# Performance work log

Measured on AMD Instinct MI355X. Metric: run time of the kernel, lower is better.

Reference implementation:

```python
import jax, jax.numpy as jnp
import numpy as np

V, E, H, Z, T = 8185, 353, 191, 13, 25
START = 19


def _lstm(x, h, c, k, rk, b):
    # Keras LSTMCell: gates ordered i, f, g(candidate), o
    gates = x @ k + h @ rk + b                      # (B, 4H)
    i, f, g, o = jnp.split(gates, 4, axis=-1)
    c_new = jax.nn.sigmoid(f) * c + jax.nn.sigmoid(i) * jnp.tanh(g)
    h_new = jax.nn.sigmoid(o) * jnp.tanh(c_new)
    return h_new, c_new


def setup_inputs() -> dict:
    key = jax.random.key(0)
    ks = jax.random.split(key, 18)
    B = 256
    s = 0.05
    inp = {
        "inputs": jax.random.randint(ks[0], (B, T), 0, V),
        "epsilon": jax.random.normal(ks[1], (Z,), jnp.float32),
        "emb": jax.random.normal(ks[2], (V, E), jnp.float32) * s,
        "inf_k": jax.random.normal(ks[3], (E, 4 * H), jnp.float32) * s,
        "inf_rk": jax.random.normal(ks[4], (H, 4 * H), jnp.float32) * s,
        "inf_b": jnp.zeros((4 * H,), jnp.float32),
        "mu_w": jax.random.normal(ks[5], (H, Z), jnp.float32) * s,
        "mu_b": jnp.zeros((Z,), jnp.float32),
        "sig_w": jax.random.normal(ks[6], (H, Z), jnp.float32) * s,
        "sig_b": jnp.zeros((Z,), jnp.float32),
        "init_w": jax.random.normal(ks[7], (Z, H), jnp.float32) * s,
        "init_b": jnp.zeros((H,), jnp.float32),
        "gen_k": jax.random.normal(ks[8], (E, 4 * H), jnp.float32) * s,
        "gen_rk": jax.random.normal(ks[9], (H, 4 * H), jnp.float32) * s,
        "gen_b": jnp.zeros((4 * H,), jnp.float32),
        "out_w": jax.random.normal(ks[10], (H, V), jnp.float32) * s,
        "out_b": jnp.zeros((V,), jnp.float32),
    }
    return inp


def reference(inputs, epsilon, emb, inf_k, inf_rk, inf_b, mu_w, mu_b,
              sig_w, sig_b, init_w, init_b, gen_k, gen_rk, gen_b,
              out_w, out_b):
    B = inputs.shape[0]
    # ----- encoder (inference LSTM over the full sequence) -----
    inf_emb = emb[inputs]                             # (B, T, E)

    def enc_step(carry, x_t):
        h, c = carry
        h, c = _lstm(x_t, h, c, inf_k, inf_rk, inf_b)
        return (h, c), None

    h0 = jnp.zeros((B, H), emb.dtype)
    (h_enc, _), _ = jax.lax.scan(enc_step, (h0, h0),
                                 jnp.swapaxes(inf_emb, 0, 1))  # scan over T

    mu = h_enc @ mu_w + mu_b                          # (B, Z)
    sigma = h_enc @ sig_w + sig_b                     # (B, Z)
    z = mu + epsilon * sigma                          # shared epsilon (Z,)

    init_state = z @ init_w + init_b                  # (B, H)
    emb0 = jnp.broadcast_to(emb[START], (B, E))       # start token embedding

    def dec_step(carry, _):
        h, c, x = carry
        h, c = _lstm(x, h, c, gen_k, gen_rk, gen_b)
        logits = h @ out_w + out_b                    # (B, V)
        new_ind = jnp.argmax(logits, axis=-1)         # (B,)
        x_next = emb[new_ind]                         # (B, E)
        return (h, c, x_next), logits

    _, logits_seq = jax.lax.scan(dec_step, (init_state, init_state, emb0),
                                 None, length=T)      # (T, B, V)
    return jnp.swapaxes(logits_seq, 0, 1)             # (B, T, V)
```

## Files before the change

kernel.cpp:

```cpp
#include <hip/hip_runtime.h>
#include <math.h>

#define V_  8185
#define E_  353
#define H_  191
#define FH_ 764
#define Z_  13
#define T_  25
#define START_ 19
#define VP_ 8192
#define NT_ 32

__device__ __forceinline__ float sigf(float x) { return 1.0f / (1.0f + expf(-x)); }

__global__ __launch_bounds__(256) void pad_w_kernel(const float* __restrict__ src,
                                                    float* __restrict__ dst) {
  int i = blockIdx.x * 256 + threadIdx.x;
  if (i >= H_ * VP_) return;
  int k = i >> 13;
  int j = i & (VP_ - 1);
  dst[i] = (j < V_) ? src[(size_t)k * V_ + j] : 0.0f;
}

__global__ __launch_bounds__(256) void gemm_ew(const float* __restrict__ emb,
                                               const float* __restrict__ W,
                                               float* __restrict__ C, int M,
                                               const int* __restrict__ inputs,
                                               int mode, int B) {
  __shared__ __align__(16) float AT[E_ * 16];
  const int tid = threadIdx.x;
  const int n0 = blockIdx.x * 256;
  const int m0 = blockIdx.y * 16;
  for (int i = tid; i < 16 * E_; i += 256) {
    int r = i / E_, k = i - r * E_;
    int m = m0 + r;
    float v = 0.0f;
    if (m < M) {
      int row;
      if (mode == 0) row = m;
      else { int t = m / B, b = m - t * B; row = inputs[b * T_ + t]; }
      v = emb[(size_t)row * E_ + k];
    }
    AT[k * 16 + r] = v;
  }
  __syncthreads();
  const int lane = tid & 63;
  const int w4 = (tid >> 6) * 4;
  const int j = n0 + lane * 4;
  if (j >= FH_) return;
  float4 c0 = {0,0,0,0}, c1 = {0,0,0,0}, c2 = {0,0,0,0}, c3 = {0,0,0,0};
  const float* wc = W + j;
  const float* at = AT + w4;
  for (int k = 0; k < E_; ++k) {
    float4 wv = *(const float4*)(wc + (size_t)k * FH_);
    float4 a  = *(const float4*)(at + k * 16);
    c0.x = fmaf(a.x, wv.x, c0.x); c0.y = fmaf(a.x, wv.y, c0.y);
    c0.z = fmaf(a.x, wv.z, c0.z); c0.w = fmaf(a.x, wv.w, c0.w);
    c1.x = fmaf(a.y, wv.x, c1.x); c1.y = fmaf(a.y, wv.y, c1.y);
    c1.z = fmaf(a.y, wv.z, c1.z); c1.w = fmaf(a.y, wv.w, c1.w);
    c2.x = fmaf(a.z, wv.x, c2.x); c2.y = fmaf(a.z, wv.y, c2.y);
    c2.z = fmaf(a.z, wv.z, c2.z); c2.w = fmaf(a.z, wv.w, c2.w);
    c3.x = fmaf(a.w, wv.x, c3.x); c3.y = fmaf(a.w, wv.y, c3.y);
    c3.z = fmaf(a.w, wv.z, c3.z); c3.w = fmaf(a.w, wv.w, c3.w);
  }
  const int mb = m0 + w4;
  if (mb + 0 < M) *(float4*)(C + (size_t)(mb + 0) * FH_ + j) = c0;
  if (mb + 1 < M) *(float4*)(C + (size_t)(mb + 1) * FH_ + j) = c1;
  if (mb + 2 < M) *(float4*)(C + (size_t)(mb + 2) * FH_ + j) = c2;
  if (mb + 3 < M) *(float4*)(C + (size_t)(mb + 3) * FH_ + j) = c3;
}

__global__ __launch_bounds__(256) void lstm_step(const float* __restrict__ xk,
                                                 const float* __restrict__ rk,
                                                 const float* __restrict__ bias,
                                                 const float* __restrict__ h_in,
                                                 const float* __restrict__ c_in,
                                                 float* __restrict__ h_out,
                                                 float* __restrict__ c_out,
                                                 const float* __restrict__ pmax,
                                                 const int* __restrict__ pidx,
                                                 int mode, int first) {
  __shared__ float hs[16 * H_];
  __shared__ float xs[16 * 32];
  __shared__ float bs[32];
  __shared__ int   tk[16];
  __shared__ float pv[16 * NT_];
  __shared__ int   pi[16 * NT_];
  __shared__ float gb[32 * 16];

  const int tid = threadIdx.x;
  const int c0 = blockIdx.x * 8;
  const int m0 = blockIdx.y * 16;

  if (mode) {
    if (first) {
      if (tid < 16) tk[tid] = START_;
    } else {
      for (int i = tid; i < 16 * NT_; i += 256) {
        int row = i >> 5, s = i & (NT_ - 1);
        pv[i] = pmax[(size_t)(m0 + row) * NT_ + s];
        pi[i] = pidx[(size_t)(m0 + row) * NT_ + s];
      }
      __syncthreads();
      if (tid < 16) {
        float bv = pv[tid * NT_]; int bi = pi[tid * NT_];
        for (int s = 1; s < NT_; ++s) {
          float v = pv[tid * NT_ + s]; int ii = pi[tid * NT_ + s];
          if (v > bv || (v == bv && ii < bi)) { bv = v; bi = ii; }
        }
        tk[tid] = bi;
      }
    }
    __syncthreads();
  }

  for (int i = tid; i < 16 * H_; i += 256) hs[i] = h_in[(size_t)m0 * H_ + i];
  for (int i = tid; i < 16 * 32; i += 256) {
    int row = i >> 5, q = i & 31;
    int jj = c0 + (q & 7);
    int jg = jj + H_ * (q >> 3);
    float xv = 0.0f;
    if (jj < H_) {
      const float* xrow = mode ? (xk + (size_t)tk[row] * FH_)
                               : (xk + (size_t)(m0 + row) * FH_);
      xv = xrow[jg];
    }
    xs[i] = xv;
  }
  if (tid < 32) {
    int jj = c0 + (tid & 7);
    bs[tid] = (jj < H_) ? bias[jj + H_ * (tid >> 3)] : 0.0f;
  }
  __syncthreads();

  const int q = tid & 31, rg = tid >> 5;
  const int jj = c0 + (q & 7);
  const int jg = jj + H_ * (q >> 3);
  float a0 = 0.0f, a1 = 0.0f;
  if (jj < H_) {
    const float* rkp = rk + jg;
    const float* h0p = hs + rg * H_;
    const float* h1p = hs + (rg + 8) * H_;
    for (int k = 0; k < H_; ++k) {
      float wv = rkp[(size_t)k * FH_];
      a0 = fmaf(h0p[k], wv, a0);
      a1 = fmaf(h1p[k], wv, a1);
    }
  }
  gb[q * 16 + rg] = a0;
  gb[q * 16 + rg + 8] = a1;
  __syncthreads();

  if (tid < 128) {
    int cc = tid & 7, row = tid >> 3;
    int jc = c0 + cc;
    if (jc < H_) {
      float gi = gb[(cc      ) * 16 + row] + xs[row * 32 + cc      ] + bs[cc];
      float gf = gb[( 8 + cc ) * 16 + row] + xs[row * 32 +  8 + cc ] + bs[ 8 + cc];
      float gg = gb[(16 + cc ) * 16 + row] + xs[row * 32 + 16 + cc ] + bs[16 + cc];
      float go = gb[(24 + cc ) * 16 + row] + xs[row * 32 + 24 + cc ] + bs[24 + cc];
      float co = c_in[(size_t)(m0 + row) * H_ + jc];
      float cn = sigf(gf) * co + sigf(gi) * tanhf(gg);
      float hn = sigf(go) * tanhf(cn);
      c_out[(size_t)(m0 + row) * H_ + jc] = cn;
      h_out[(size_t)(m0 + row) * H_ + jc] = hn;
    }
  }
}

__global__ __launch_bounds__(256) void logits_argmax(const float* __restrict__ h,
                                                     const float* __restrict__ wp,
                                                     const float* __restrict__ ob,
                                                     float* __restrict__ out, int t,
                                                     float* __restrict__ pmax,
                                                     int* __restrict__ pidx) {
  __shared__ __align__(16) float AT[H_ * 16];
  const int tid = threadIdx.x;
  const int n0 = blockIdx.x * 256;
  const int m0 = blockIdx.y * 16;
  for (int i = tid; i < 16 * H_; i += 256) {
    int r = i / H_, k = i - r * H_;
    AT[k * 16 + r] = h[(size_t)m0 * H_ + i];
  }
  __syncthreads();
  const int lane = tid & 63;
  const int w4 = (tid >> 6) * 4;
  const int j = n0 + lane * 4;
  float4 c0 = {0,0,0,0}, c1 = {0,0,0,0}, c2 = {0,0,0,0}, c3 = {0,0,0,0};
  const float* wc = wp + j;
  const float* at = AT + w4;
  for (int k = 0; k < H_; ++k) {
    float4 wv = *(const float4*)(wc + (size_t)k * VP_);
    float4 a  = *(const float4*)(at + k * 16);
    c0.x = fmaf(a.x, wv.x, c0.x); c0.y = fmaf(a.x, wv.y, c0.y);
    c0.z = fmaf(a.x, wv.z, c0.z); c0.w = fmaf(a.x, wv.w, c0.w);
    c1.x = fmaf(a.y, wv.x, c1.x); c1.y = fmaf(a.y, wv.y, c1.y);
    c1.z = fmaf(a.y, wv.z, c1.z); c1.w = fmaf(a.y, wv.w, c1.w);
    c2.x = fmaf(a.z, wv.x, c2.x); c2.y = fmaf(a.z, wv.y, c2.y);
    c2.z = fmaf(a.z, wv.z, c2.z); c2.w = fmaf(a.z, wv.w, c2.w);
    c3.x = fmaf(a.w, wv.x, c3.x); c3.y = fmaf(a.w, wv.y, c3.y);
    c3.z = fmaf(a.w, wv.z, c3.z); c3.w = fmaf(a.w, wv.w, c3.w);
  }
  float bias[4];
#pragma unroll
  for (int u = 0; u < 4; ++u) bias[u] = (j + u < V_) ? ob[j + u] : 0.0f;
  float4 accs[4] = {c0, c1, c2, c3};
  const int b0 = m0 + w4;
#pragma unroll
  for (int r = 0; r < 4; ++r) {
    const int b = b0 + r;
    float v[4] = {accs[r].x + bias[0], accs[r].y + bias[1],
                  accs[r].z + bias[2], accs[r].w + bias[3]};
    float* orow = out + ((size_t)b * T_ + t) * V_ + j;
#pragma unroll
    for (int u = 0; u < 4; ++u)
      if (j + u < V_) orow[u] = v[u];
    float bv = -INFINITY; int bi = 0;
#pragma unroll
    for (int u = 0; u < 4; ++u)
      if (j + u < V_ && v[u] > bv) { bv = v[u]; bi = j + u; }
#pragma unroll
    for (int off = 1; off < 64; off <<= 1) {
      float ov = __shfl_xor(bv, off, 64);
      int   oi = __shfl_xor(bi, off, 64);
      if (ov > bv || (ov == bv && oi < bi)) { bv = ov; bi = oi; }
    }
    if (lane == 0) {
      pmax[(size_t)b * NT_ + blockIdx.x] = bv;
      pidx[(size_t)b * NT_ + blockIdx.x] = bi;
    }
  }
}

__global__ __launch_bounds__(64) void latent_k(const float* __restrict__ h,
                                               const float* __restrict__ eps,
                                               const float* __restrict__ mu_w,
                                               const float* __restrict__ mu_b,
                                               const float* __restrict__ sig_w,
                                               const float* __restrict__ sig_b,
                                               const float* __restrict__ iw,
                                               const float* __restrict__ ib,
                                               float* __restrict__ h0,
                                               float* __restrict__ c0) {
  __shared__ float zs[4 * Z_];
  const int tid = threadIdx.x;
  const int m0 = blockIdx.x * 4;
  if (tid < 4 * Z_) {
    int row = tid / Z_, qz = tid - row * Z_;
    const float* hr = h + (size_t)(m0 + row) * H_;
    float mu = mu_b[qz], sg = sig_b[qz];
    for (int k = 0; k < H_; ++k) {
      float hv = hr[k];
      mu = fmaf(hv, mu_w[k * Z_ + qz], mu);
      sg = fmaf(hv, sig_w[k * Z_ + qz], sg);
    }
    zs[tid] = mu + eps[qz] * sg;
  }
  __syncthreads();
  for (int i = tid; i < 4 * H_; i += 64) {
    int row = i / H_, col = i - row * H_;
    float acc = ib[col];
#pragma unroll
    for (int qz = 0; qz < Z_; ++qz)
      acc = fmaf(zs[row * Z_ + qz], iw[qz * H_ + col], acc);
    h0[(size_t)(m0 + row) * H_ + col] = acc;
    c0[(size_t)(m0 + row) * H_ + col] = acc;
  }
}

extern "C" void kernel_launch(void* const* d_in, const int* in_sizes, int n_in,
                              void* d_out, int out_size, void* d_ws, size_t ws_size,
                              hipStream_t stream) {
  const int*   inputs = (const int*)  d_in[0];
  const float* eps    = (const float*)d_in[1];
  const float* emb    = (const float*)d_in[2];
  const float* inf_k  = (const float*)d_in[3];
  const float* inf_rk = (const float*)d_in[4];
  const float* inf_b  = (const float*)d_in[5];
  const float* mu_w   = (const float*)d_in[6];
  const float* mu_b   = (const float*)d_in[7];
  const float* sig_w  = (const float*)d_in[8];
  const float* sig_b  = (const float*)d_in[9];
  const float* init_w = (const float*)d_in[10];
  const float* init_b = (const float*)d_in[11];
  const float* gen_k  = (const float*)d_in[12];
  const float* gen_rk = (const float*)d_in[13];
  const float* gen_b  = (const float*)d_in[14];
  const float* out_w  = (const float*)d_in[15];
  const float* out_b  = (const float*)d_in[16];
  float* out = (float*)d_out;

  const int B = in_sizes[0] / T_;
  const int BH = B * H_;

  float* ws = (float*)d_ws;
  size_t off = 0;
  float* EK = ws + off; off += (size_t)V_ * FH_;
  float* XK = ws + off; off += (size_t)T_ * B * FH_;
  float* WP = ws + off; off += (size_t)H_ * VP_;
  float* hbase = ws + off; off += (size_t)8 * BH;
  float* he[2] = {hbase + 0 * BH, hbase + 2 * BH};
  float* ce[2] = {hbase + 1 * BH, hbase + 3 * BH};
  float* hd[2] = {hbase + 4 * BH, hbase + 6 * BH};
  float* cd[2] = {hbase + 5 * BH, hbase + 7 * BH};
  float* pmax = ws + off; off += (size_t)B * NT_;
  int*   pidx = (int*)(ws + off); off += (size_t)B * NT_;

  hipMemsetAsync(hbase, 0, (size_t)2 * BH * sizeof(float), stream);

  pad_w_kernel<<<(H_ * VP_ + 255) / 256, 256, 0, stream>>>(out_w, WP);
  gemm_ew<<<dim3(3, (V_ + 15) / 16), 256, 0, stream>>>(emb, gen_k, EK, V_, nullptr, 0, B);
  gemm_ew<<<dim3(3, (T_ * B) / 16), 256, 0, stream>>>(emb, inf_k, XK, T_ * B, inputs, 1, B);

  for (int t = 0; t < T_; ++t) {
    lstm_step<<<dim3(24, B / 16), 256, 0, stream>>>(
        XK + (size_t)t * B * FH_, inf_rk, inf_b,
        he[t & 1], ce[t & 1], he[(t + 1) & 1], ce[(t + 1) & 1],
        nullptr, nullptr, 0, 0);
  }

  latent_k<<<B / 4, 64, 0, stream>>>(he[T_ & 1], eps, mu_w, mu_b, sig_w, sig_b,
                                     init_w, init_b, hd[0], cd[0]);

  for (int t = 0; t < T_; ++t) {
    lstm_step<<<dim3(24, B / 16), 256, 0, stream>>>(
        EK, gen_rk, gen_b,
        hd[t & 1], cd[t & 1], hd[(t + 1) & 1], cd[(t + 1) & 1],
        pmax, pidx, 1, (t == 0) ? 1 : 0);
    logits_argmax<<<dim3(NT_, B / 16), 256, 0, stream>>>(
        hd[(t + 1) & 1], WP, out_b, out, t, pmax, pidx);
  }
}
```

Measured before the change: 1.889 ms.

## Fuse encoder timesteps and latent into one persistent kernel; retile GEMMs

Replaces the 25 per-step encoder launches and the latent kernel with a single encoder_all kernel. Each block runs the whole encoder recurrence for two batch rows with h/c kept in shared memory, then computes mu/sigma/z and the decoder initial state. The two embedding GEMMs merge into one launch with 32-row tiles. The logits/argmax kernel is retiled to 32 rows by 128 columns with nontemporal stores, and the partial-argmax count grows to 64. This removes launch overhead and global round-trips in the encoder. The cost is only 128 small blocks, each re-streaming the full recurrent weight matrix every step.

```diff
diff --git a/kernel.cpp b/kernel.cpp
--- a/kernel.cpp
+++ b/kernel.cpp
@@ -9,7 +9,7 @@
 #define T_  25
 #define START_ 19
 #define VP_ 8192
-#define NT_ 32
+#define NT_ 64
 
 __device__ __forceinline__ float sigf(float x) { return 1.0f / (1.0f + expf(-x)); }
 
@@ -22,55 +22,148 @@
   dst[i] = (j < V_) ? src[(size_t)k * V_ + j] : 0.0f;
 }
 
+#define FMA4(A, S) \
+  A.x = fmaf(S, wv.x, A.x); A.y = fmaf(S, wv.y, A.y); \
+  A.z = fmaf(S, wv.z, A.z); A.w = fmaf(S, wv.w, A.w);
+
 __global__ __launch_bounds__(256) void gemm_ew(const float* __restrict__ emb,
-                                               const float* __restrict__ W,
-                                               float* __restrict__ C, int M,
+                                               const float* __restrict__ Wa,
+                                               float* __restrict__ Ca, int Ma,
+                                               const float* __restrict__ Wb,
+                                               float* __restrict__ Cb, int Mb,
                                                const int* __restrict__ inputs,
-                                               int mode, int B) {
-  __shared__ __align__(16) float AT[E_ * 16];
+                                               int B, int yA) {
+  __shared__ __align__(16) float AT[32 * E_];
   const int tid = threadIdx.x;
   const int n0 = blockIdx.x * 256;
-  const int m0 = blockIdx.y * 16;
-  for (int i = tid; i < 16 * E_; i += 256) {
-    int r = i / E_, k = i - r * E_;
+  int yb = blockIdx.y;
+  const float* W; float* C; int M; int gatherB;
+  if (yb < yA) { W = Wa; C = Ca; M = Ma; gatherB = 0; }
+  else { yb -= yA; W = Wb; C = Cb; M = Mb; gatherB = 1; }
+  const int m0 = yb * 32;
+
+  for (int i = tid; i < 32 * E_; i += 256) {
+    int r = i & 31, k = i >> 5;
     int m = m0 + r;
     float v = 0.0f;
     if (m < M) {
       int row;
-      if (mode == 0) row = m;
-      else { int t = m / B, b = m - t * B; row = inputs[b * T_ + t]; }
+      if (gatherB == 0) row = m;
+      else { int tt = m / B, b = m - tt * B; row = inputs[b * T_ + tt]; }
       v = emb[(size_t)row * E_ + k];
     }
-    AT[k * 16 + r] = v;
-  }
-  __syncthreads();
+    AT[i] = v;
+  }
+  __syncthreads();
+
   const int lane = tid & 63;
-  const int w4 = (tid >> 6) * 4;
+  const int w8 = (tid >> 6) * 8;
   const int j = n0 + lane * 4;
   if (j >= FH_) return;
-  float4 c0 = {0,0,0,0}, c1 = {0,0,0,0}, c2 = {0,0,0,0}, c3 = {0,0,0,0};
+  float4 a0 = {0,0,0,0}, a1 = {0,0,0,0}, a2 = {0,0,0,0}, a3 = {0,0,0,0};
+  float4 a4 = {0,0,0,0}, a5 = {0,0,0,0}, a6 = {0,0,0,0}, a7 = {0,0,0,0};
   const float* wc = W + j;
-  const float* at = AT + w4;
+  const float* at = AT + w8;
+#pragma unroll 2
   for (int k = 0; k < E_; ++k) {
     float4 wv = *(const float4*)(wc + (size_t)k * FH_);
-    float4 a  = *(const float4*)(at + k * 16);
-    c0.x = fmaf(a.x, wv.x, c0.x); c0.y = fmaf(a.x, wv.y, c0.y);
-    c0.z = fmaf(a.x, wv.z, c0.z); c0.w = fmaf(a.x, wv.w, c0.w);
-    c1.x = fmaf(a.y, wv.x, c1.x); c1.y = fmaf(a.y, wv.y, c1.y);
-    c1.z = fmaf(a.y, wv.z, c1.z); c1.w = fmaf(a.y, wv.w, c1.w);
-    c2.x = fmaf(a.z, wv.x, c2.x); c2.y = fmaf(a.z, wv.y, c2.y);
-    c2.z = fmaf(a.z, wv.z, c2.z); c2.w = fmaf(a.z, wv.w, c2.w);
-    c3.x = fmaf(a.w, wv.x, c3.x); c3.y = fmaf(a.w, wv.y, c3.y);
-    c3.z = fmaf(a.w, wv.z, c3.z); c3.w = fmaf(a.w, wv.w, c3.w);
-  }
-  const int mb = m0 + w4;
-  if (mb + 0 < M) *(float4*)(C + (size_t)(mb + 0) * FH_ + j) = c0;
-  if (mb + 1 < M) *(float4*)(C + (size_t)(mb + 1) * FH_ + j) = c1;
-  if (mb + 2 < M) *(float4*)(C + (size_t)(mb + 2) * FH_ + j) = c2;
-  if (mb + 3 < M) *(float4*)(C + (size_t)(mb + 3) * FH_ + j) = c3;
-}
-
-__global__ __launch_bounds__(256) void lstm_step(const float* __restrict__ xk,
+    float4 r03 = *(const float4*)(at + k * 32);
+    float4 r47 = *(const float4*)(at + k * 32 + 4);
+    FMA4(a0, r03.x) FMA4(a1, r03.y) FMA4(a2, r03.z) FMA4(a3, r03.w)
+    FMA4(a4, r47.x) FMA4(a5, r47.y) FMA4(a6, r47.z) FMA4(a7, r47.w)
+  }
+  const int mb = m0 + w8;
+  float4 accs[8] = {a0, a1, a2, a3, a4, a5, a6, a7};
+#pragma unroll
+  for (int r = 0; r < 8; ++r)
+    if (mb + r < M) *(float4*)(C + (size_t)(mb + r) * FH_ + j) = accs[r];
+}
+
+__global__ __launch_bounds__(192) void encoder_all(
+    const float* __restrict__ xk,
+    const float* __restrict__ rk,
+    const float* __restrict__ bias,
+    const float* __restrict__ eps,
+    const float* __restrict__ mu_w, const float* __restrict__ mu_b,
+    const float* __restrict__ sig_w, const float* __restrict__ sig_b,
+    const float* __restrict__ iw, const float* __restrict__ ib,
+    float* __restrict__ h0o, float* __restrict__ c0o, int B) {
+  __shared__ float h[2][H_], c[2][H_];
+  __shared__ __align__(16) float g[2][FH_];
+  __shared__ float zs[2][Z_];
+  const int tid = threadIdx.x;
+  const int b0 = blockIdx.x * 2;
+
+  if (tid < H_) {
+    h[0][tid] = 0.0f; h[1][tid] = 0.0f;
+    c[0][tid] = 0.0f; c[1][tid] = 0.0f;
+  }
+  const bool act = tid < (FH_ / 4);
+  const int q4 = tid * 4;
+  float4 b4 = act ? *(const float4*)(bias + q4) : make_float4(0, 0, 0, 0);
+  const float* rkq = rk + q4;
+  __syncthreads();
+
+  for (int t = 0; t < T_; ++t) {
+    if (act) {
+      const float* xr = xk + ((size_t)t * B + b0) * FH_ + q4;
+      float4 x0 = *(const float4*)(xr);
+      float4 x1 = *(const float4*)(xr + FH_);
+      float4 a0 = {0,0,0,0}, a1 = {0,0,0,0};
+#pragma unroll 4
+      for (int k = 0; k < H_; ++k) {
+        float4 wv = *(const float4*)(rkq + (size_t)k * FH_);
+        float h0v = h[0][k], h1v = h[1][k];
+        a0.x = fmaf(h0v, wv.x, a0.x); a0.y = fmaf(h0v, wv.y, a0.y);
+        a0.z = fmaf(h0v, wv.z, a0.z); a0.w = fmaf(h0v, wv.w, a0.w);
+        a1.x = fmaf(h1v, wv.x, a1.x); a1.y = fmaf(h1v, wv.y, a1.y);
+        a1.z = fmaf(h1v, wv.z, a1.z); a1.w = fmaf(h1v, wv.w, a1.w);
+      }
+      float4 g0 = make_float4(a0.x + x0.x + b4.x, a0.y + x0.y + b4.y,
+                              a0.z + x0.z + b4.z, a0.w + x0.w + b4.w);
+      float4 g1 = make_float4(a1.x + x1.x + b4.x, a1.y + x1.y + b4.y,
+                              a1.z + x1.z + b4.z, a1.w + x1.w + b4.w);
+      *(float4*)(&g[0][q4]) = g0;
+      *(float4*)(&g[1][q4]) = g1;
+    }
+    __syncthreads();
+    if (tid < H_) {
+#pragma unroll
+      for (int r = 0; r < 2; ++r) {
+        float gi = g[r][tid], gf = g[r][H_ + tid];
+        float gg = g[r][2 * H_ + tid], go = g[r][3 * H_ + tid];
+        float cn = sigf(gf) * c[r][tid] + sigf(gi) * tanhf(gg);
+        c[r][tid] = cn;
+        h[r][tid] = sigf(go) * tanhf(cn);
+      }
+    }
+    __syncthreads();
+  }
+
+  if (tid < 2 * Z_) {
+    int r = tid / Z_, zq = tid - r * Z_;
+    float mu = mu_b[zq], sg = sig_b[zq];
+    for (int k = 0; k < H_; ++k) {
+      float hv = h[r][k];
+      mu = fmaf(hv, mu_w[k * Z_ + zq], mu);
+      sg = fmaf(hv, sig_w[k * Z_ + zq], sg);
+    }
+    zs[r][zq] = mu + eps[zq] * sg;
+  }
+  __syncthreads();
+  if (tid < H_) {
+#pragma unroll
+    for (int r = 0; r < 2; ++r) {
+      float acc = ib[tid];
+#pragma unroll
+      for (int z = 0; z < Z_; ++z) acc = fmaf(zs[r][z], iw[z * H_ + tid], acc);
+      h0o[(size_t)(b0 + r) * H_ + tid] = acc;
+      c0o[(size_t)(b0 + r) * H_ + tid] = acc;
+    }
+  }
+}
+
+__global__ __launch_bounds__(256) void lstm_step(const float* __restrict__ ek,
                                                  const float* __restrict__ rk,
                                                  const float* __restrict__ bias,
                                                  const float* __restrict__ h_in,
@@ -79,7 +172,7 @@
                                                  float* __restrict__ c_out,
                                                  const float* __restrict__ pmax,
                                                  const int* __restrict__ pidx,
-                                                 int mode, int first) {
+                                                 int first) {
   __shared__ float hs[16 * H_];
   __shared__ float xs[16 * 32];
   __shared__ float bs[32];
@@ -92,27 +185,25 @@
   const int c0 = blockIdx.x * 8;
   const int m0 = blockIdx.y * 16;
 
-  if (mode) {
-    if (first) {
-      if (tid < 16) tk[tid] = START_;
-    } else {
-      for (int i = tid; i < 16 * NT_; i += 256) {
-        int row = i >> 5, s = i & (NT_ - 1);
-        pv[i] = pmax[(size_t)(m0 + row) * NT_ + s];
-        pi[i] = pidx[(size_t)(m0 + row) * NT_ + s];
+  if (first) {
+    if (tid < 16) tk[tid] = START_;
+  } else {
+    for (int i = tid; i < 16 * NT_; i += 256) {
+      int row = i / NT_, s = i - row * NT_;
+      pv[i] = pmax[(size_t)(m0 + row) * NT_ + s];
+      pi[i] = pidx[(size_t)(m0 + row) * NT_ + s];
+    }
+    __syncthreads();
+    if (tid < 16) {
+      float bv = pv[tid * NT_]; int bi = pi[tid * NT_];
+      for (int s = 1; s < NT_; ++s) {
+        float v = pv[tid * NT_ + s]; int ii = pi[tid * NT_ + s];
+        if (v > bv || (v == bv && ii < bi)) { bv = v; bi = ii; }
       }
-      __syncthreads();
-      if (tid < 16) {
-        float bv = pv[tid * NT_]; int bi = pi[tid * NT_];
-        for (int s = 1; s < NT_; ++s) {
-          float v = pv[tid * NT_ + s]; int ii = pi[tid * NT_ + s];
-          if (v > bv || (v == bv && ii < bi)) { bv = v; bi = ii; }
-        }
-        tk[tid] = bi;
-      }
-    }
-    __syncthreads();
-  }
+      tk[tid] = bi;
+    }
+  }
+  __syncthreads();
 
   for (int i = tid; i < 16 * H_; i += 256) hs[i] = h_in[(size_t)m0 * H_ + i];
   for (int i = tid; i < 16 * 32; i += 256) {
@@ -120,11 +211,7 @@
     int jj = c0 + (q & 7);
     int jg = jj + H_ * (q >> 3);
     float xv = 0.0f;
-    if (jj < H_) {
-      const float* xrow = mode ? (xk + (size_t)tk[row] * FH_)
-                               : (xk + (size_t)(m0 + row) * FH_);
-      xv = xrow[jg];
-    }
+    if (jj < H_) xv = ek[(size_t)tk[row] * FH_ + jg];
     xs[i] = xv;
   }
   if (tid < 32) {
@@ -174,51 +261,58 @@
                                                      float* __restrict__ out, int t,
                                                      float* __restrict__ pmax,
                                                      int* __restrict__ pidx) {
-  __shared__ __align__(16) float AT[H_ * 16];
+  __shared__ __align__(16) float AT[32 * H_];
   const int tid = threadIdx.x;
-  const int n0 = blockIdx.x * 256;
-  const int m0 = blockIdx.y * 16;
-  for (int i = tid; i < 16 * H_; i += 256) {
-    int r = i / H_, k = i - r * H_;
-    AT[k * 16 + r] = h[(size_t)m0 * H_ + i];
-  }
-  __syncthreads();
+  const int n0 = blockIdx.x * 128;
+  const int m0 = blockIdx.y * 32;
+  for (int i = tid; i < 32 * H_; i += 256) {
+    int r = i & 31, k = i >> 5;
+    AT[i] = h[(size_t)(m0 + r) * H_ + k];
+  }
+  __syncthreads();
+
   const int lane = tid & 63;
-  const int w4 = (tid >> 6) * 4;
-  const int j = n0 + lane * 4;
-  float4 c0 = {0,0,0,0}, c1 = {0,0,0,0}, c2 = {0,0,0,0}, c3 = {0,0,0,0};
+  const int w8 = (tid >> 6) * 8;
+  const int j = n0 + lane * 2;
+  float2 acc[8];
+#pragma unroll
+  for (int r = 0; r < 8; ++r) acc[r] = make_float2(0.0f, 0.0f);
   const float* wc = wp + j;
-  const float* at = AT + w4;
+  const float* at = AT + w8;
+#pragma unroll 2
   for (int k = 0; k < H_; ++k) {
-    float4 wv = *(const float4*)(wc + (size_t)k * VP_);
-    float4 a  = *(const float4*)(at + k * 16);
-    c0.x = fmaf(a.x, wv.x, c0.x); c0.y = fmaf(a.x, wv.y, c0.y);
-    c0.z = fmaf(a.x, wv.z, c0.z); c0.w = fmaf(a.x, wv.w, c0.w);
-    c1.x = fmaf(a.y, wv.x, c1.x); c1.y = fmaf(a.y, wv.y, c1.y);
-    c1.z = fmaf(a.y, wv.z, c1.z); c1.w = fmaf(a.y, wv.w, c1.w);
-    c2.x = fmaf(a.z, wv.x, c2.x); c2.y = fmaf(a.z, wv.y, c2.y);
-    c2.z = fmaf(a.z, wv.z, c2.z); c2.w = fmaf(a.z, wv.w, c2.w);
-    c3.x = fmaf(a.w, wv.x, c3.x); c3.y = fmaf(a.w, wv.y, c3.y);
-    c3.z = fmaf(a.w, wv.z, c3.z); c3.w = fmaf(a.w, wv.w, c3.w);
-  }
-  float bias[4];
-#pragma unroll
-  for (int u = 0; u < 4; ++u) bias[u] = (j + u < V_) ? ob[j + u] : 0.0f;
-  float4 accs[4] = {c0, c1, c2, c3};
-  const int b0 = m0 + w4;
-#pragma unroll
-  for (int r = 0; r < 4; ++r) {
-    const int b = b0 + r;
-    float v[4] = {accs[r].x + bias[0], accs[r].y + bias[1],
-                  accs[r].z + bias[2], accs[r].w + bias[3]};
+    float2 wv = *(const float2*)(wc + (size_t)k * VP_);
+    float4 r03 = *(const float4*)(at + k * 32);
+    float4 r47 = *(const float4*)(at + k * 32 + 4);
+    acc[0].x = fmaf(r03.x, wv.x, acc[0].x); acc[0].y = fmaf(r03.x, wv.y, acc[0].y);
+    acc[1].x = fmaf(r03.y, wv.x, acc[1].x); acc[1].y = fmaf(r03.y, wv.y, acc[1].y);
+    acc[2].x = fmaf(r03.z, wv.x, acc[2].x); acc[2].y = fmaf(r03.z, wv.y, acc[2].y);
+    acc[3].x = fmaf(r03.w, wv.x, acc[3].x); acc[3].y = fmaf(r03.w, wv.y, acc[3].y);
+    acc[4].x = fmaf(r47.x, wv.x, acc[4].x); acc[4].y = fmaf(r47.x, wv.y, acc[4].y);
+    acc[5].x = fmaf(r47.y, wv.x, acc[5].x); acc[5].y = fmaf(r47.y, wv.y, acc[5].y);
+    acc[6].x = fmaf(r47.z, wv.x, acc[6].x); acc[6].y = fmaf(r47.z, wv.y, acc[6].y);
+    acc[7].x = fmaf(r47.w, wv.x, acc[7].x); acc[7].y = fmaf(r47.w, wv.y, acc[7].y);
+  }
+
+  float bj0 = (j < V_) ? ob[j] : 0.0f;
+  float bj1 = (j + 1 < V_) ? ob[j + 1] : 0.0f;
+  const bool tile_full = (n0 + 128 <= V_);
+#pragma unroll
+  for (int r = 0; r < 8; ++r) {
+    const int b = m0 + w8 + r;
+    float v0 = acc[r].x + bj0;
+    float v1 = acc[r].y + bj1;
     float* orow = out + ((size_t)b * T_ + t) * V_ + j;
-#pragma unroll
-    for (int u = 0; u < 4; ++u)
-      if (j + u < V_) orow[u] = v[u];
+    if (tile_full) {
+      __builtin_nontemporal_store(v0, orow);
+      __builtin_nontemporal_store(v1, orow + 1);
+    } else {
+      if (j < V_)     orow[0] = v0;
+      if (j + 1 < V_) orow[1] = v1;
+    }
     float bv = -INFINITY; int bi = 0;
-#pragma unroll
-    for (int u = 0; u < 4; ++u)
-      if (j + u < V_ && v[u] > bv) { bv = v[u]; bi = j + u; }
+    if (j < V_)                 { bv = v0; bi = j; }
+    if (j + 1 < V_ && v1 > bv)  { bv = v1; bi = j + 1; }
 #pragma unroll
     for (int off = 1; off < 64; off <<= 1) {
       float ov = __shfl_xor(bv, off, 64);
@@ -229,42 +323,6 @@
       pmax[(size_t)b * NT_ + blockIdx.x] = bv;
       pidx[(size_t)b * NT_ + blockIdx.x] = bi;
     }
-  }
-}
-
-__global__ __launch_bounds__(64) void latent_k(const float* __restrict__ h,
-                                               const float* __restrict__ eps,
-                                               const float* __restrict__ mu_w,
-                                               const float* __restrict__ mu_b,
-                                               const float* __restrict__ sig_w,
-                                               const float* __restrict__ sig_b,
-                                               const float* __restrict__ iw,
-                                               const float* __restrict__ ib,
-                                               float* __restrict__ h0,
-                                               float* __restrict__ c0) {
-  __shared__ float zs[4 * Z_];
-  const int tid = threadIdx.x;
-  const int m0 = blockIdx.x * 4;
-  if (tid < 4 * Z_) {
-    int row = tid / Z_, qz = tid - row * Z_;
-    const float* hr = h + (size_t)(m0 + row) * H_;
-    float mu = mu_b[qz], sg = sig_b[qz];
-    for (int k = 0; k < H_; ++k) {
-      float hv = hr[k];
-      mu = fmaf(hv, mu_w[k * Z_ + qz], mu);
-      sg = fmaf(hv, sig_w[k * Z_ + qz], sg);
-    }
-    zs[tid] = mu + eps[qz] * sg;
-  }
-  __syncthreads();
-  for (int i = tid; i < 4 * H_; i += 64) {
-    int row = i / H_, col = i - row * H_;
-    float acc = ib[col];
-#pragma unroll
-    for (int qz = 0; qz < Z_; ++qz)
-      acc = fmaf(zs[row * Z_ + qz], iw[qz * H_ + col], acc);
-    h0[(size_t)(m0 + row) * H_ + col] = acc;
-    c0[(size_t)(m0 + row) * H_ + col] = acc;
   }
 }
 
@@ -298,36 +356,29 @@
   float* EK = ws + off; off += (size_t)V_ * FH_;
   float* XK = ws + off; off += (size_t)T_ * B * FH_;
   float* WP = ws + off; off += (size_t)H_ * VP_;
-  float* hbase = ws + off; off += (size_t)8 * BH;
-  float* he[2] = {hbase + 0 * BH, hbase + 2 * BH};
-  float* ce[2] = {hbase + 1 * BH, hbase + 3 * BH};
-  float* hd[2] = {hbase + 4 * BH, hbase + 6 * BH};
-  float* cd[2] = {hbase + 5 * BH, hbase + 7 * BH};
+  float* hbase = ws + off; off += (size_t)4 * BH;
+  float* hd[2] = {hbase + 0 * BH, hbase + 2 * BH};
+  float* cd[2] = {hbase + 1 * BH, hbase + 3 * BH};
   float* pmax = ws + off; off += (size_t)B * NT_;
   int*   pidx = (int*)(ws + off); off += (size_t)B * NT_;
 
-  hipMemsetAsync(hbase, 0, (size_t)2 * BH * sizeof(float), stream);
-
   pad_w_kernel<<<(H_ * VP_ + 255) / 256, 256, 0, stream>>>(out_w, WP);
-  gemm_ew<<<dim3(3, (V_ + 15) / 16), 256, 0, stream>>>(emb, gen_k, EK, V_, nullptr, 0, B);
-  gemm_ew<<<dim3(3, (T_ * B) / 16), 256, 0, stream>>>(emb, inf_k, XK, T_ * B, inputs, 1, B);
-
-  for (int t = 0; t < T_; ++t) {
-    lstm_step<<<dim3(24, B / 16), 256, 0, stream>>>(
-        XK + (size_t)t * B * FH_, inf_rk, inf_b,
-        he[t & 1], ce[t & 1], he[(t + 1) & 1], ce[(t + 1) & 1],
-        nullptr, nullptr, 0, 0);
-  }
-
-  latent_k<<<B / 4, 64, 0, stream>>>(he[T_ & 1], eps, mu_w, mu_b, sig_w, sig_b,
-                                     init_w, init_b, hd[0], cd[0]);
+  const int yEK = (V_ + 31) / 32;
+  const int yXK = (T_ * B + 31) / 32;
+  gemm_ew<<<dim3(3, yEK + yXK), 256, 0, stream>>>(emb, gen_k, EK, V_,
+                                                  inf_k, XK, T_ * B,
+                                                  inputs, B, yEK);
+
+  encoder_all<<<B / 2, 192, 0, stream>>>(XK, inf_rk, inf_b, eps,
+                                         mu_w, mu_b, sig_w, sig_b,
+                                         init_w, init_b, hd[0], cd[0], B);
 
   for (int t = 0; t < T_; ++t) {
     lstm_step<<<dim3(24, B / 16), 256, 0, stream>>>(
         EK, gen_rk, gen_b,
         hd[t & 1], cd[t & 1], hd[(t + 1) & 1], cd[(t + 1) & 1],
-        pmax, pidx, 1, (t == 0) ? 1 : 0);
-    logits_argmax<<<dim3(NT_, B / 16), 256, 0, stream>>>(
+        pmax, pidx, (t == 0) ? 1 : 0);
+    logits_argmax<<<dim3(NT_, B / 32), 256, 0, stream>>>(
         hd[(t + 1) & 1], WP, out_b, out, t, pmax, pidx);
   }
 }
```

After: 2.478 ms. 1.31x slower.

## Fuse encoder LSTM steps and latent projection into one persistent kernel with grid barrier

Applied to the files above, without the earlier changes.

Replaces the 25 per-timestep encoder lstm_step launches and the latent kernel with a single persistent kernel that loops over time, synchronising all blocks with a software grid barrier built on atomics. Each block keeps its slice of the recurrent weights in shared memory and its cell state in registers across steps, so weights are not reloaded and the c buffers are dropped. The latent mu/sigma/init projection runs at the end inside the same kernel. This removes launch overhead and repeated weight loads, but it relies on all 384 blocks being co-resident, or the barrier deadlocks, and it adds barrier spin latency at every step.

```diff
diff --git a/kernel.cpp b/kernel.cpp
--- a/kernel.cpp
+++ b/kernel.cpp
@@ -10,8 +10,28 @@
 #define START_ 19
 #define VP_ 8192
 #define NT_ 32
+#define HS_ 192
+#define NB_ 384
 
 __device__ __forceinline__ float sigf(float x) { return 1.0f / (1.0f + expf(-x)); }
+
+__device__ __forceinline__ void grid_barrier(unsigned* cnt, unsigned* gen) {
+  __syncthreads();
+  if (threadIdx.x == 0) {
+    __threadfence();
+    unsigned g = __hip_atomic_load(gen, __ATOMIC_RELAXED, __HIP_MEMORY_SCOPE_AGENT);
+    unsigned a = __hip_atomic_fetch_add(cnt, 1u, __ATOMIC_ACQ_REL, __HIP_MEMORY_SCOPE_AGENT);
+    if (a == NB_ - 1u) {
+      __hip_atomic_store(cnt, 0u, __ATOMIC_RELAXED, __HIP_MEMORY_SCOPE_AGENT);
+      __hip_atomic_store(gen, g + 1u, __ATOMIC_RELEASE, __HIP_MEMORY_SCOPE_AGENT);
+    } else {
+      while (__hip_atomic_load(gen, __ATOMIC_ACQUIRE, __HIP_MEMORY_SCOPE_AGENT) == g)
+        __builtin_amdgcn_s_sleep(1);
+    }
+    __threadfence();
+  }
+  __syncthreads();
+}
 
 __global__ __launch_bounds__(256) void pad_w_kernel(const float* __restrict__ src,
                                                     float* __restrict__ dst) {
@@ -70,6 +90,135 @@
   if (mb + 3 < M) *(float4*)(C + (size_t)(mb + 3) * FH_ + j) = c3;
 }
 
+__global__ __launch_bounds__(256) void encoder_persist(
+    const float* __restrict__ xk,
+    const float* __restrict__ rk,
+    const float* __restrict__ bias,
+    const float* __restrict__ eps,
+    const float* __restrict__ mu_w, const float* __restrict__ mu_b,
+    const float* __restrict__ sig_w, const float* __restrict__ sig_b,
+    const float* __restrict__ iw, const float* __restrict__ ib,
+    float* __restrict__ h0o, float* __restrict__ c0o,
+    float* __restrict__ hb0, float* __restrict__ hb1,
+    unsigned* __restrict__ bar, int B) {
+  __shared__ float rks[H_ * 32];
+  __shared__ __align__(16) float hs[16 * HS_];
+  __shared__ float xs[16 * 32];
+  __shared__ float bs[32];
+  __shared__ float gb[32 * 16];
+  __shared__ float zz[16 * Z_];
+
+  const int tid = threadIdx.x;
+  const int c0 = blockIdx.x * 8;
+  const int m0 = blockIdx.y * 16;
+
+  for (int i = tid; i < H_ * 32; i += 256) {
+    int k = i >> 5, qq = i & 31;
+    int j2 = c0 + (qq & 7);
+    rks[i] = (j2 < H_) ? rk[(size_t)k * FH_ + j2 + H_ * (qq >> 3)] : 0.0f;
+  }
+  if (tid < 32) {
+    int j2 = c0 + (tid & 7);
+    bs[tid] = (j2 < H_) ? bias[j2 + H_ * (tid >> 3)] : 0.0f;
+  }
+
+  const int q = tid & 31, r2 = tid >> 5;
+  const int jj = c0 + (q & 7);
+  const int pc = tid & 7, prow = tid >> 3;
+  float creg = 0.0f;
+
+  float* hbuf[2] = {hb0, hb1};
+  __syncthreads();
+
+  for (int t = 0; t < T_; ++t) {
+    if (t > 0) {
+      const float* hsrc = hbuf[t & 1] + (size_t)m0 * H_;
+      for (int i = tid; i < 16 * H_; i += 256) {
+        int r = i / H_, k = i - r * H_;
+        hs[r * HS_ + k] = hsrc[i];
+      }
+    }
+    for (int i = tid; i < 16 * 32; i += 256) {
+      int row = i >> 5, qq = i & 31;
+      int j2 = c0 + (qq & 7);
+      float xv = 0.0f;
+      if (j2 < H_)
+        xv = xk[((size_t)t * B + m0 + row) * FH_ + j2 + H_ * (qq >> 3)];
+      xs[i] = xv;
+    }
+    __syncthreads();
+
+    float a0 = 0.0f, a1 = 0.0f;
+    if (t > 0 && jj < H_) {
+      const float* h0p = hs + r2 * HS_;
+      const float* h1p = hs + (r2 + 8) * HS_;
+      int k = 0;
+      for (; k < 188; k += 4) {
+        float4 h0v = *(const float4*)(h0p + k);
+        float4 h1v = *(const float4*)(h1p + k);
+        float w0 = rks[(k + 0) * 32 + q], w1 = rks[(k + 1) * 32 + q];
+        float w2 = rks[(k + 2) * 32 + q], w3 = rks[(k + 3) * 32 + q];
+        a0 = fmaf(h0v.x, w0, a0); a1 = fmaf(h1v.x, w0, a1);
+        a0 = fmaf(h0v.y, w1, a0); a1 = fmaf(h1v.y, w1, a1);
+        a0 = fmaf(h0v.z, w2, a0); a1 = fmaf(h1v.z, w2, a1);
+        a0 = fmaf(h0v.w, w3, a0); a1 = fmaf(h1v.w, w3, a1);
+      }
+      for (; k < H_; ++k) {
+        float wv = rks[k * 32 + q];
+        a0 = fmaf(h0p[k], wv, a0);
+        a1 = fmaf(h1p[k], wv, a1);
+      }
+    }
+    gb[q * 16 + r2] = a0;
+    gb[q * 16 + r2 + 8] = a1;
+    __syncthreads();
+
+    if (tid < 128) {
+      int jc = c0 + pc;
+      if (jc < H_) {
+        float gi = gb[(pc     ) * 16 + prow] + xs[prow * 32 + pc     ] + bs[pc];
+        float gf = gb[( 8 + pc) * 16 + prow] + xs[prow * 32 +  8 + pc] + bs[ 8 + pc];
+        float gg = gb[(16 + pc) * 16 + prow] + xs[prow * 32 + 16 + pc] + bs[16 + pc];
+        float go = gb[(24 + pc) * 16 + prow] + xs[prow * 32 + 24 + pc] + bs[24 + pc];
+        float cn = sigf(gf) * creg + sigf(gi) * tanhf(gg);
+        creg = cn;
+        hbuf[(t + 1) & 1][(size_t)(m0 + prow) * H_ + jc] = sigf(go) * tanhf(cn);
+      }
+    }
+    grid_barrier(bar, bar + 1);
+  }
+
+  if (blockIdx.x == 0) {
+    const float* hf = hbuf[T_ & 1] + (size_t)m0 * H_;
+    for (int i = tid; i < 16 * H_; i += 256) {
+      int r = i / H_, k = i - r * H_;
+      hs[r * HS_ + k] = hf[i];
+    }
+    __syncthreads();
+    if (tid < 16 * Z_) {
+      int row = tid / Z_, zq = tid - row * Z_;
+      const float* hr = hs + row * HS_;
+      float mu = mu_b[zq], sg = sig_b[zq];
+      for (int k = 0; k < H_; ++k) {
+        float hv = hr[k];
+        mu = fmaf(hv, mu_w[k * Z_ + zq], mu);
+        sg = fmaf(hv, sig_w[k * Z_ + zq], sg);
+      }
+      zz[tid] = mu + eps[zq] * sg;
+    }
+    __syncthreads();
+    for (int i = tid; i < 16 * H_; i += 256) {
+      int row = i / H_, col = i - row * H_;
+      float acc = ib[col];
+#pragma unroll
+      for (int z = 0; z < Z_; ++z)
+        acc = fmaf(zz[row * Z_ + z], iw[z * H_ + col], acc);
+      h0o[(size_t)(m0 + row) * H_ + col] = acc;
+      c0o[(size_t)(m0 + row) * H_ + col] = acc;
+    }
+  }
+}
+
 __global__ __launch_bounds__(256) void lstm_step(const float* __restrict__ xk,
                                                  const float* __restrict__ rk,
                                                  const float* __restrict__ bias,
@@ -229,42 +378,6 @@
       pmax[(size_t)b * NT_ + blockIdx.x] = bv;
       pidx[(size_t)b * NT_ + blockIdx.x] = bi;
     }
-  }
-}
-
-__global__ __launch_bounds__(64) void latent_k(const float* __restrict__ h,
-                                               const float* __restrict__ eps,
-                                               const float* __restrict__ mu_w,
-                                               const float* __restrict__ mu_b,
-                                               const float* __restrict__ sig_w,
-                                               const float* __restrict__ sig_b,
-                                               const float* __restrict__ iw,
-                                               const float* __restrict__ ib,
-                                               float* __restrict__ h0,
-                                               float* __restrict__ c0) {
-  __shared__ float zs[4 * Z_];
-  const int tid = threadIdx.x;
-  const int m0 = blockIdx.x * 4;
-  if (tid < 4 * Z_) {
-    int row = tid / Z_, qz = tid - row * Z_;
-    const float* hr = h + (size_t)(m0 + row) * H_;
-    float mu = mu_b[qz], sg = sig_b[qz];
-    for (int k = 0; k < H_; ++k) {
-      float hv = hr[k];
-      mu = fmaf(hv, mu_w[k * Z_ + qz], mu);
-      sg = fmaf(hv, sig_w[k * Z_ + qz], sg);
-    }
-    zs[tid] = mu + eps[qz] * sg;
-  }
-  __syncthreads();
-  for (int i = tid; i < 4 * H_; i += 64) {
-    int row = i / H_, col = i - row * H_;
-    float acc = ib[col];
-#pragma unroll
-    for (int qz = 0; qz < Z_; ++qz)
-      acc = fmaf(zs[row * Z_ + qz], iw[qz * H_ + col], acc);
-    h0[(size_t)(m0 + row) * H_ + col] = acc;
-    c0[(size_t)(m0 + row) * H_ + col] = acc;
   }
 }
 
@@ -298,29 +411,24 @@
   float* EK = ws + off; off += (size_t)V_ * FH_;
   float* XK = ws + off; off += (size_t)T_ * B * FH_;
   float* WP = ws + off; off += (size_t)H_ * VP_;
-  float* hbase = ws + off; off += (size_t)8 * BH;
-  float* he[2] = {hbase + 0 * BH, hbase + 2 * BH};
-  float* ce[2] = {hbase + 1 * BH, hbase + 3 * BH};
-  float* hd[2] = {hbase + 4 * BH, hbase + 6 * BH};
-  float* cd[2] = {hbase + 5 * BH, hbase + 7 * BH};
+  float* hbase = ws + off; off += (size_t)4 * BH;
+  float* hd[2] = {hbase + 0 * BH, hbase + 2 * BH};
+  float* cd[2] = {hbase + 1 * BH, hbase + 3 * BH};
+  float* hb0 = ws + off; off += (size_t)BH;
+  float* hb1 = ws + off; off += (size_t)BH;
   float* pmax = ws + off; off += (size_t)B * NT_;
   int*   pidx = (int*)(ws + off); off += (size_t)B * NT_;
-
-  hipMemsetAsync(hbase, 0, (size_t)2 * BH * sizeof(float), stream);
+  unsigned* bar = (unsigned*)(ws + off); off += 2;
+
+  hipMemsetAsync(bar, 0, 2 * sizeof(unsigned), stream);
 
   pad_w_kernel<<<(H_ * VP_ + 255) / 256, 256, 0, stream>>>(out_w, WP);
   gemm_ew<<<dim3(3, (V_ + 15) / 16), 256, 0, stream>>>(emb, gen_k, EK, V_, nullptr, 0, B);
   gemm_ew<<<dim3(3, (T_ * B) / 16), 256, 0, stream>>>(emb, inf_k, XK, T_ * B, inputs, 1, B);
 
-  for (int t = 0; t < T_; ++t) {
-    lstm_step<<<dim3(24, B / 16), 256, 0, stream>>>(
-        XK + (size_t)t * B * FH_, inf_rk, inf_b,
-        he[t & 1], ce[t & 1], he[(t + 1) & 1], ce[(t + 1) & 1],
-        nullptr, nullptr, 0, 0);
-  }
-
-  latent_k<<<B / 4, 64, 0, stream>>>(he[T_ & 1], eps, mu_w, mu_b, sig_w, sig_b,
-                                     init_w, init_b, hd[0], cd[0]);
+  encoder_persist<<<dim3(24, B / 16), 256, 0, stream>>>(
+      XK, inf_rk, inf_b, eps, mu_w, mu_b, sig_w, sig_b,
+      init_w, init_b, hd[0], cd[0], hb0, hb1, bar, B);
 
   for (int t = 0; t < T_; ++t) {
     lstm_step<<<dim3(24, B / 16), 256, 0, stream>>>(
```

New measurement: 3.143 ms. 66.3% more time.

## Transpose recurrent weights into LDS and retile logits kernel to 32x128 blocks

Applied to the files above, without the earlier changes.

Adds a one-time transpose of both recurrent weight matrices into a padded k-contiguous layout. Each lstm_step block stages its 32 weight columns into shared memory and runs the recurrent dot product with float4 reads of h, replacing strided global loads. The logits/argmax kernel now uses 32-row by 128-column tiles (64 column tiles instead of 32), so each weight load is reused across more batch rows. The argmax partial buffers and the reduction widen to match. This costs more shared memory per lstm block and an extra setup kernel.

```diff
diff --git a/kernel.cpp b/kernel.cpp
--- a/kernel.cpp
+++ b/kernel.cpp
@@ -9,7 +9,8 @@
 #define T_  25
 #define START_ 19
 #define VP_ 8192
-#define NT_ 32
+#define NTL 64
+#define RKS 192
 
 __device__ __forceinline__ float sigf(float x) { return 1.0f / (1.0f + expf(-x)); }
 
@@ -20,6 +21,17 @@
   int k = i >> 13;
   int j = i & (VP_ - 1);
   dst[i] = (j < V_) ? src[(size_t)k * V_ + j] : 0.0f;
+}
+
+__global__ __launch_bounds__(256) void transpose_rk(const float* __restrict__ rkA,
+                                                    const float* __restrict__ rkB,
+                                                    float* __restrict__ dst) {
+  int i = blockIdx.x * 256 + threadIdx.x;
+  if (i >= 2 * FH_ * RKS) return;
+  int w = i / (FH_ * RKS), rem = i - w * (FH_ * RKS);
+  int col4 = rem / RKS, k = rem - col4 * RKS;
+  const float* src = w ? rkB : rkA;
+  dst[i] = (k < H_) ? src[(size_t)k * FH_ + col4] : 0.0f;
 }
 
 __global__ __launch_bounds__(256) void gemm_ew(const float* __restrict__ emb,
@@ -71,7 +83,7 @@
 }
 
 __global__ __launch_bounds__(256) void lstm_step(const float* __restrict__ xk,
-                                                 const float* __restrict__ rk,
+                                                 const float* __restrict__ rkT,
                                                  const float* __restrict__ bias,
                                                  const float* __restrict__ h_in,
                                                  const float* __restrict__ c_in,
@@ -80,12 +92,13 @@
                                                  const float* __restrict__ pmax,
                                                  const int* __restrict__ pidx,
                                                  int mode, int first) {
-  __shared__ float hs[16 * H_];
+  __shared__ float rks[32][193];
+  __shared__ __align__(16) float hs[16][RKS];
   __shared__ float xs[16 * 32];
   __shared__ float bs[32];
   __shared__ int   tk[16];
-  __shared__ float pv[16 * NT_];
-  __shared__ int   pi[16 * NT_];
+  __shared__ float pv[16 * NTL];
+  __shared__ int   pi[16 * NTL];
   __shared__ float gb[32 * 16];
 
   const int tid = threadIdx.x;
@@ -96,16 +109,16 @@
     if (first) {
       if (tid < 16) tk[tid] = START_;
     } else {
-      for (int i = tid; i < 16 * NT_; i += 256) {
-        int row = i >> 5, s = i & (NT_ - 1);
-        pv[i] = pmax[(size_t)(m0 + row) * NT_ + s];
-        pi[i] = pidx[(size_t)(m0 + row) * NT_ + s];
+      for (int i = tid; i < 16 * NTL; i += 256) {
+        int row = i >> 6, s = i & (NTL - 1);
+        pv[i] = pmax[(size_t)(m0 + row) * NTL + s];
+        pi[i] = pidx[(size_t)(m0 + row) * NTL + s];
       }
       __syncthreads();
       if (tid < 16) {
-        float bv = pv[tid * NT_]; int bi = pi[tid * NT_];
-        for (int s = 1; s < NT_; ++s) {
-          float v = pv[tid * NT_ + s]; int ii = pi[tid * NT_ + s];
+        float bv = pv[tid * NTL]; int bi = pi[tid * NTL];
+        for (int s = 1; s < NTL; ++s) {
+          float v = pv[tid * NTL + s]; int ii = pi[tid * NTL + s];
           if (v > bv || (v == bv && ii < bi)) { bv = v; bi = ii; }
         }
         tk[tid] = bi;
@@ -114,7 +127,18 @@
     __syncthreads();
   }
 
-  for (int i = tid; i < 16 * H_; i += 256) hs[i] = h_in[(size_t)m0 * H_ + i];
+  for (int i = tid; i < 32 * 48; i += 256) {
+    int qq = i / 48, kq = (i - qq * 48) * 4;
+    int jj2 = c0 + (qq & 7), g = qq >> 3;
+    float4 v = {0, 0, 0, 0};
+    if (jj2 < H_) v = *(const float4*)(rkT + (size_t)(jj2 + H_ * g) * RKS + kq);
+    rks[qq][kq]     = v.x; rks[qq][kq + 1] = v.y;
+    rks[qq][kq + 2] = v.z; rks[qq][kq + 3] = v.w;
+  }
+  for (int i = tid; i < 16 * H_; i += 256) {
+    int r = i / H_, k = i - r * H_;
+    hs[r][k] = h_in[(size_t)m0 * H_ + i];
+  }
   for (int i = tid; i < 16 * 32; i += 256) {
     int row = i >> 5, q = i & 31;
     int jj = c0 + (q & 7);
@@ -135,14 +159,23 @@
 
   const int q = tid & 31, rg = tid >> 5;
   const int jj = c0 + (q & 7);
-  const int jg = jj + H_ * (q >> 3);
   float a0 = 0.0f, a1 = 0.0f;
   if (jj < H_) {
-    const float* rkp = rk + jg;
-    const float* h0p = hs + rg * H_;
-    const float* h1p = hs + (rg + 8) * H_;
-    for (int k = 0; k < H_; ++k) {
-      float wv = rkp[(size_t)k * FH_];
+    const float* rr  = rks[q];
+    const float* h0p = hs[rg];
+    const float* h1p = hs[rg + 8];
+    int k = 0;
+    for (; k < 188; k += 4) {
+      float4 h0v = *(const float4*)(h0p + k);
+      float4 h1v = *(const float4*)(h1p + k);
+      float w0 = rr[k], w1 = rr[k + 1], w2 = rr[k + 2], w3 = rr[k + 3];
+      a0 = fmaf(h0v.x, w0, a0); a1 = fmaf(h1v.x, w0, a1);
+      a0 = fmaf(h0v.y, w1, a0); a1 = fmaf(h1v.y, w1, a1);
+      a0 = fmaf(h0v.z, w2, a0); a1 = fmaf(h1v.z, w2, a1);
+      a0 = fmaf(h0v.w, w3, a0); a1 = fmaf(h1v.w, w3, a1);
+    }
+    for (; k < H_; ++k) {
+      float wv = rr[k];
       a0 = fmaf(h0p[k], wv, a0);
       a1 = fmaf(h1p[k], wv, a1);
     }
@@ -174,60 +207,65 @@
                                                      float* __restrict__ out, int t,
                                                      float* __restrict__ pmax,
                                                      int* __restrict__ pidx) {
-  __shared__ __align__(16) float AT[H_ * 16];
+  __shared__ __align__(16) float AT[H_ * 36];
   const int tid = threadIdx.x;
-  const int n0 = blockIdx.x * 256;
-  const int m0 = blockIdx.y * 16;
-  for (int i = tid; i < 16 * H_; i += 256) {
+  const int n0 = blockIdx.x * 128;
+  const int m0 = blockIdx.y * 32;
+  for (int i = tid; i < 32 * H_; i += 256) {
     int r = i / H_, k = i - r * H_;
-    AT[k * 16 + r] = h[(size_t)m0 * H_ + i];
-  }
-  __syncthreads();
-  const int lane = tid & 63;
-  const int w4 = (tid >> 6) * 4;
-  const int j = n0 + lane * 4;
-  float4 c0 = {0,0,0,0}, c1 = {0,0,0,0}, c2 = {0,0,0,0}, c3 = {0,0,0,0};
+    AT[k * 36 + r] = h[(size_t)m0 * H_ + i];
+  }
+  __syncthreads();
+
+  const int cq = tid & 31;
+  const int ro = tid >> 5;
+  const int j = n0 + cq * 4;
+  float4 acc[4] = {{0,0,0,0},{0,0,0,0},{0,0,0,0},{0,0,0,0}};
   const float* wc = wp + j;
-  const float* at = AT + w4;
+  const float* at = AT + ro * 4;
   for (int k = 0; k < H_; ++k) {
     float4 wv = *(const float4*)(wc + (size_t)k * VP_);
-    float4 a  = *(const float4*)(at + k * 16);
-    c0.x = fmaf(a.x, wv.x, c0.x); c0.y = fmaf(a.x, wv.y, c0.y);
-    c0.z = fmaf(a.x, wv.z, c0.z); c0.w = fmaf(a.x, wv.w, c0.w);
-    c1.x = fmaf(a.y, wv.x, c1.x); c1.y = fmaf(a.y, wv.y, c1.y);
-    c1.z = fmaf(a.y, wv.z, c1.z); c1.w = fmaf(a.y, wv.w, c1.w);
-    c2.x = fmaf(a.z, wv.x, c2.x); c2.y = fmaf(a.z, wv.y, c2.y);
-    c2.z = fmaf(a.z, wv.z, c2.z); c2.w = fmaf(a.z, wv.w, c2.w);
-    c3.x = fmaf(a.w, wv.x, c3.x); c3.y = fmaf(a.w, wv.y, c3.y);
-    c3.z = fmaf(a.w, wv.z, c3.z); c3.w = fmaf(a.w, wv.w, c3.w);
-  }
-  float bias[4];
-#pragma unroll
-  for (int u = 0; u < 4; ++u) bias[u] = (j + u < V_) ? ob[j + u] : 0.0f;
-  float4 accs[4] = {c0, c1, c2, c3};
-  const int b0 = m0 + w4;
-#pragma unroll
-  for (int r = 0; r < 4; ++r) {
-    const int b = b0 + r;
-    float v[4] = {accs[r].x + bias[0], accs[r].y + bias[1],
-                  accs[r].z + bias[2], accs[r].w + bias[3]};
+    float4 a  = *(const float4*)(at + k * 36);
+    acc[0].x = fmaf(a.x, wv.x, acc[0].x); acc[0].y = fmaf(a.x, wv.y, acc[0].y);
+    acc[0].z = fmaf(a.x, wv.z, acc[0].z); acc[0].w = fmaf(a.x, wv.w, acc[0].w);
+    acc[1].x = fmaf(a.y, wv.x, acc[1].x); acc[1].y = fmaf(a.y, wv.y, acc[1].y);
+    acc[1].z = fmaf(a.y, wv.z, acc[1].z); acc[1].w = fmaf(a.y, wv.w, acc[1].w);
+    acc[2].x = fmaf(a.z, wv.x, acc[2].x); acc[2].y = fmaf(a.z, wv.y, acc[2].y);
+    acc[2].z = fmaf(a.z, wv.z, acc[2].z); acc[2].w = fmaf(a.z, wv.w, acc[2].w);
+    acc[3].x = fmaf(a.w, wv.x, acc[3].x); acc[3].y = fmaf(a.w, wv.y, acc[3].y);
+    acc[3].z = fmaf(a.w, wv.z, acc[3].z); acc[3].w = fmaf(a.w, wv.w, acc[3].w);
+  }
+
+  float bias4[4];
+#pragma unroll
+  for (int u = 0; u < 4; ++u) bias4[u] = (j + u < V_) ? ob[j + u] : 0.0f;
+  const bool tile_full = (n0 + 128 <= V_);
+#pragma unroll
+  for (int rr = 0; rr < 4; ++rr) {
+    const int b = m0 + ro * 4 + rr;
+    float v[4] = {acc[rr].x + bias4[0], acc[rr].y + bias4[1],
+                  acc[rr].z + bias4[2], acc[rr].w + bias4[3]};
     float* orow = out + ((size_t)b * T_ + t) * V_ + j;
-#pragma unroll
-    for (int u = 0; u < 4; ++u)
-      if (j + u < V_) orow[u] = v[u];
+    if (tile_full) {
+      orow[0] = v[0]; orow[1] = v[1]; orow[2] = v[2]; orow[3] = v[3];
+    } else {
+#pragma unroll
+      for (int u = 0; u < 4; ++u)
+        if (j + u < V_) orow[u] = v[u];
+    }
     float bv = -INFINITY; int bi = 0;
 #pragma unroll
     for (int u = 0; u < 4; ++u)
       if (j + u < V_ && v[u] > bv) { bv = v[u]; bi = j + u; }
 #pragma unroll
-    for (int off = 1; off < 64; off <<= 1) {
+    for (int off = 1; off < 32; off <<= 1) {
       float ov = __shfl_xor(bv, off, 64);
       int   oi = __shfl_xor(bi, off, 64);
       if (ov > bv || (ov == bv && oi < bi)) { bv = ov; bi = oi; }
     }
-    if (lane == 0) {
-      pmax[(size_t)b * NT_ + blockIdx.x] = bv;
-      pidx[(size_t)b * NT_ + blockIdx.x] = bi;
+    if ((tid & 31) == 0) {
+      pmax[(size_t)b * NTL + blockIdx.x] = bv;
+      pidx[(size_t)b * NTL + blockIdx.x] = bi;
     }
   }
 }
@@ -298,23 +336,27 @@
   float* EK = ws + off; off += (size_t)V_ * FH_;
   float* XK = ws + off; off += (size_t)T_ * B * FH_;
   float* WP = ws + off; off += (size_t)H_ * VP_;
+  float* rkT = ws + off; off += (size_t)2 * FH_ * RKS;
   float* hbase = ws + off; off += (size_t)8 * BH;
   float* he[2] = {hbase + 0 * BH, hbase + 2 * BH};
   float* ce[2] = {hbase + 1 * BH, hbase + 3 * BH};
   float* hd[2] = {hbase + 4 * BH, hbase + 6 * BH};
   float* cd[2] = {hbase + 5 * BH, hbase + 7 * BH};
-  float* pmax = ws + off; off += (size_t)B * NT_;
-  int*   pidx = (int*)(ws + off); off += (size_t)B * NT_;
+  float* pmax = ws + off; off += (size_t)B * NTL;
+  int*   pidx = (int*)(ws + off); off += (size_t)B * NTL;
+  float* rkT_inf = rkT;
+  float* rkT_gen = rkT + (size_t)FH_ * RKS;
 
   hipMemsetAsync(hbase, 0, (size_t)2 * BH * sizeof(float), stream);
 
   pad_w_kernel<<<(H_ * VP_ + 255) / 256, 256, 0, stream>>>(out_w, WP);
+  transpose_rk<<<(2 * FH_ * RKS + 255) / 256, 256, 0, stream>>>(inf_rk, gen_rk, rkT);
   gemm_ew<<<dim3(3, (V_ + 15) / 16), 256, 0, stream>>>(emb, gen_k, EK, V_, nullptr, 0, B);
   gemm_ew<<<dim3(3, (T_ * B) / 16), 256, 0, stream>>>(emb, inf_k, XK, T_ * B, inputs, 1, B);
 
   for (int t = 0; t < T_; ++t) {
     lstm_step<<<dim3(24, B / 16), 256, 0, stream>>>(
-        XK + (size_t)t * B * FH_, inf_rk, inf_b,
+        XK + (size_t)t * B * FH_, rkT_inf, inf_b,
         he[t & 1], ce[t & 1], he[(t + 1) & 1], ce[(t + 1) & 1],
         nullptr, nullptr, 0, 0);
   }
@@ -324,10 +366,10 @@
 
   for (int t = 0; t < T_; ++t) {
     lstm_step<<<dim3(24, B / 16), 256, 0, stream>>>(
-        EK, gen_rk, gen_b,
+        EK, rkT_gen, gen_b,
         hd[t & 1], cd[t & 1], hd[(t + 1) & 1], cd[(t + 1) & 1],
         pmax, pidx, 1, (t == 0) ? 1 : 0);
-    logits_argmax<<<dim3(NT_, B / 16), 256, 0, stream>>>(
+    logits_argmax<<<dim3(NTL, B / 32), 256, 0, stream>>>(
         hd[(t + 1) & 1], WP, out_b, out, t, pmax, pidx);
   }
 }
```

Result: faster. 1.724 ms (-8.8%).
